# Kernel tuning notes

Hardware: AMD Instinct MI355X
Metric: run time of the kernel (lower is better)

The kernel has to match this reference:

```python
import jax, jax.numpy as jnp
import numpy as np

HEADS = 16
EPS = 1e-6

def _rmsnorm(x, g):
    # x: (..., d); norm = ||x||_2 * d^-0.5 (matches torch.norm-based RMSNorm)
    d = x.shape[-1]
    nrm = jnp.linalg.norm(x, axis=-1, keepdims=True) * (d ** -0.5)
    return x / (nrm + EPS) * g

def _rope(x, cos, sin):
    # x: (b,n,h,d) -> complex pairs over last dim; cos/sin: (1,n,1,d//2)
    b, n, h, d = x.shape
    xr = x.reshape(b, n, h, d // 2, 2)
    re, im = xr[..., 0], xr[..., 1]
    out_re = re * cos - im * sin
    out_im = re * sin + im * cos
    return jnp.stack([out_re, out_im], axis=-1).reshape(b, n, h, d)

def setup_inputs() -> dict:
    key = jax.random.key(0)
    ks = jax.random.split(key, 8)
    b, n, dim = 4, 4096, 1024
    d = dim // HEADS
    x = jax.random.normal(ks[0], (b, n, dim), dtype=jnp.float32)
    # rope freqs as cos/sin of random angles (broadcast shape 1,n,1,d//2)
    ang = jax.random.uniform(ks[1], (1, n, 1, d // 2), dtype=jnp.float32) * (2 * np.pi)
    freqs_cos = jnp.cos(ang)
    freqs_sin = jnp.sin(ang)
    sc = dim ** -0.5
    w_qkv = jax.random.normal(ks[2], (dim, 3 * dim), dtype=jnp.float32) * sc
    g_q = jnp.ones((d,), dtype=jnp.float32)
    g_k = jnp.ones((d,), dtype=jnp.float32)
    w_proj = jax.random.normal(ks[3], (dim, dim), dtype=jnp.float32) * sc
    b_proj = jnp.zeros((dim,), dtype=jnp.float32)
    return {"x": x, "freqs_cos": freqs_cos, "freqs_sin": freqs_sin,
            "w_qkv": w_qkv, "g_q": g_q, "g_k": g_k,
            "w_proj": w_proj, "b_proj": b_proj}

def reference(x, freqs_cos, freqs_sin, w_qkv, g_q, g_k, w_proj, b_proj):
    b, n, dim = x.shape
    h = HEADS
    d = dim // h
    scale = d ** -0.5
    qkv = x @ w_qkv  # (b,n,3*dim)
    q, k, v = jnp.split(qkv, 3, axis=-1)
    q = q.reshape(b, n, h, d)
    k = k.reshape(b, n, h, d)
    v = v.reshape(b, n, h, d)
    q = _rmsnorm(q, g_q)
    k = _rmsnorm(k, g_k)
    q = _rope(q, freqs_cos, freqs_sin)
    k = _rope(k, freqs_cos, freqs_sin)
    # per-token head-mixing attention: (b,n,h,h)
    attn = jnp.einsum('bnhd,bngd->bnhg', q, k) * scale
    attn = jax.nn.softmax(attn, axis=-1)
    out = jnp.einsum('bnhg,bngd->bnhd', attn, v).reshape(b, n, dim)
    return out @ w_proj + b_proj
```

## Files before the change

### kernel.cpp

```cpp
#include <hip/hip_runtime.h>
#include <hip/hip_bf16.h>
#include <stddef.h>

#define NTOK   16384
#define SEQN   4096
#define DIM    1024
#define K3     3072
#define HEADS  16
#define HD     64

typedef __attribute__((ext_vector_type(8))) short short8;
typedef __attribute__((ext_vector_type(4))) float float4v;

static __device__ __forceinline__ unsigned short f32_to_bf16_bits(float f) {
    unsigned u = __float_as_uint(f);
    unsigned r = u + 0x7fffu + ((u >> 16) & 1u);
    return (unsigned short)(r >> 16);
}
static __device__ __forceinline__ float bf16_bits_to_f32(unsigned short h) {
    return __uint_as_float(((unsigned)h) << 16);
}

typedef const void __attribute__((address_space(1)))* gas_ptr;
typedef void __attribute__((address_space(3)))* las_ptr;
static __device__ __forceinline__ void gload_lds16(const unsigned short* g,
                                                   unsigned short* l) {
    __builtin_amdgcn_global_load_lds((gas_ptr)g, (las_ptr)l, 16, 0, 0);
}

__global__ void cvt_f32_bf16(const float4* __restrict__ in,
                             ushort4* __restrict__ out, int n4) {
    int i = blockIdx.x * blockDim.x + threadIdx.x;
    if (i < n4) {
        float4 v = in[i];
        ushort4 o;
        o.x = f32_to_bf16_bits(v.x);
        o.y = f32_to_bf16_bits(v.y);
        o.z = f32_to_bf16_bits(v.z);
        o.w = f32_to_bf16_bits(v.w);
        out[i] = o;
    }
}

__global__ void transpose_cvt(const float* __restrict__ in,
                              unsigned short* __restrict__ out,
                              int K, int N) {
    __shared__ float t[32][33];
    int n0 = blockIdx.x * 32, k0 = blockIdx.y * 32;
    int tx = threadIdx.x, ty = threadIdx.y;
    #pragma unroll
    for (int r = ty; r < 32; r += 8)
        t[r][tx] = in[(size_t)(k0 + r) * N + n0 + tx];
    __syncthreads();
    #pragma unroll
    for (int r = ty; r < 32; r += 8)
        out[(size_t)(n0 + r) * K + k0 + tx] = f32_to_bf16_bits(t[tx][r]);
}

template<int WITH_BIAS>
__global__ __launch_bounds__(256) void gemm_bf16_128(
    const unsigned short* __restrict__ A,
    const unsigned short* __restrict__ Bt,
    void* __restrict__ Cout,
    const float* __restrict__ bias,
    int M, int N, int K)
{
    __shared__ unsigned short As[128][32];
    __shared__ unsigned short Bs[128][32];

    const int tid  = threadIdx.x;
    const int wave = tid >> 6;
    const int lane = tid & 63;
    const int quad = lane >> 4;
    const int l16  = lane & 15;
    const int waveM = (wave & 1) * 64;
    const int waveN = (wave >> 1) * 64;
    const int rowBase = blockIdx.y * 128;
    const int colBase = blockIdx.x * 128;

    float4v acc[4][4];
    #pragma unroll
    for (int i = 0; i < 4; i++)
        #pragma unroll
        for (int j = 0; j < 4; j++)
            acc[i][j] = (float4v)0.0f;

    const int lrow = lane >> 2;
    const int lcol = (lane & 3) * 8;
    const unsigned short* gA = A  + (size_t)(rowBase + wave * 32 + lrow) * K + lcol;
    const unsigned short* gB = Bt + (size_t)(colBase + wave * 32 + lrow) * K + lcol;
    unsigned short* lA0 = &As[wave * 32][0];
    unsigned short* lA1 = &As[wave * 32 + 16][0];
    unsigned short* lB0 = &Bs[wave * 32][0];
    unsigned short* lB1 = &Bs[wave * 32 + 16][0];
    const size_t k16 = (size_t)16 * K;

    for (int k0 = 0; k0 < K; k0 += 32) {
        __syncthreads();
        gload_lds16(gA + k0,        lA0);
        gload_lds16(gA + k0 + k16,  lA1);
        gload_lds16(gB + k0,        lB0);
        gload_lds16(gB + k0 + k16,  lB1);
        __syncthreads();

        short8 af[4], bf[4];
        #pragma unroll
        for (int i = 0; i < 4; i++)
            af[i] = *(const short8*)&As[waveM + i * 16 + l16][quad * 8];
        #pragma unroll
        for (int j = 0; j < 4; j++)
            bf[j] = *(const short8*)&Bs[waveN + j * 16 + l16][quad * 8];

        #pragma unroll
        for (int i = 0; i < 4; i++)
            #pragma unroll
            for (int j = 0; j < 4; j++)
                acc[i][j] = __builtin_amdgcn_mfma_f32_16x16x32_bf16(
                                af[i], bf[j], acc[i][j], 0, 0, 0);
    }

    #pragma unroll
    for (int i = 0; i < 4; i++) {
        #pragma unroll
        for (int j = 0; j < 4; j++) {
            const int col = colBase + waveN + j * 16 + l16;
            #pragma unroll
            for (int r = 0; r < 4; r++) {
                const int row = rowBase + waveM + i * 16 + quad * 4 + r;
                float v = acc[i][j][r];
                if (WITH_BIAS) {
                    ((float*)Cout)[(size_t)row * N + col] = v + bias[col];
                } else {
                    ((unsigned short*)Cout)[(size_t)row * N + col] =
                        f32_to_bf16_bits(v);
                }
            }
        }
    }
}

__global__ __launch_bounds__(256) void attn_tok(
    const unsigned short* __restrict__ qkv,
    const float* __restrict__ fcos,
    const float* __restrict__ fsin,
    const float* __restrict__ gq,
    const float* __restrict__ gk,
    unsigned short* __restrict__ outb)
{
    __shared__ float qs[16][68];
    __shared__ float ks[16][68];
    __shared__ float vs[16][68];
    __shared__ float Ps[16][17];

    const int tok = blockIdx.x;
    const int tid = threadIdx.x;
    const int n   = tok & (SEQN - 1);
    const int h   = tid >> 4;
    const int l   = tid & 15;
    const int d0  = l * 4;

    const unsigned short* base = qkv + (size_t)tok * K3;
    ushort4 qu = *(const ushort4*)(base + tid * 4);
    ushort4 ku = *(const ushort4*)(base + DIM + tid * 4);
    ushort4 vu = *(const ushort4*)(base + 2 * DIM + tid * 4);

    float qx = bf16_bits_to_f32(qu.x), qy = bf16_bits_to_f32(qu.y),
          qz = bf16_bits_to_f32(qu.z), qw = bf16_bits_to_f32(qu.w);
    float kx = bf16_bits_to_f32(ku.x), ky = bf16_bits_to_f32(ku.y),
          kz = bf16_bits_to_f32(ku.z), kw = bf16_bits_to_f32(ku.w);
    float vx = bf16_bits_to_f32(vu.x), vy = bf16_bits_to_f32(vu.y),
          vz = bf16_bits_to_f32(vu.z), vw = bf16_bits_to_f32(vu.w);

    *(float4*)&vs[h][d0] = make_float4(vx, vy, vz, vw);

    float ssq = qx * qx + qy * qy + qz * qz + qw * qw;
    float ssk = kx * kx + ky * ky + kz * kz + kw * kw;
    #pragma unroll
    for (int o = 1; o < 16; o <<= 1) {
        ssq += __shfl_xor(ssq, o);
        ssk += __shfl_xor(ssk, o);
    }
    const float sq = 1.0f / (sqrtf(ssq) * 0.125f + 1e-6f);
    const float sk = 1.0f / (sqrtf(ssk) * 0.125f + 1e-6f);

    float4 g4q = *(const float4*)(gq + d0);
    float4 g4k = *(const float4*)(gk + d0);
    float qa = qx * sq * g4q.x, qb = qy * sq * g4q.y,
          qc = qz * sq * g4q.z, qd = qw * sq * g4q.w;
    float ka = kx * sk * g4k.x, kb = ky * sk * g4k.y,
          kc = kz * sk * g4k.z, kd = kw * sk * g4k.w;

    const int pi = n * (HD / 2) + l * 2;
    float c0 = fcos[pi],     s0 = fsin[pi];
    float c1 = fcos[pi + 1], s1 = fsin[pi + 1];
    *(float4*)&qs[h][d0] = make_float4(qa * c0 - qb * s0, qa * s0 + qb * c0,
                                       qc * c1 - qd * s1, qc * s1 + qd * c1);
    *(float4*)&ks[h][d0] = make_float4(ka * c0 - kb * s0, ka * s0 + kb * c0,
                                       kc * c1 - kd * s1, kc * s1 + kd * c1);
    __syncthreads();

    float s = 0.f;
    const float4* qrow = (const float4*)&qs[h][0];
    const float4* krow = (const float4*)&ks[l][0];
    #pragma unroll
    for (int t = 0; t < 16; t++) {
        float4 a = qrow[t], b = krow[t];
        s += a.x * b.x + a.y * b.y + a.z * b.z + a.w * b.w;
    }
    s *= 0.125f;

    float m = s;
    #pragma unroll
    for (int o = 1; o < 16; o <<= 1) m = fmaxf(m, __shfl_xor(m, o));
    float e = __expf(s - m);
    float sum = e;
    #pragma unroll
    for (int o = 1; o < 16; o <<= 1) sum += __shfl_xor(sum, o);
    Ps[h][l] = e / sum;
    __syncthreads();

    float ox = 0.f, oy = 0.f, oz = 0.f, ow = 0.f;
    #pragma unroll
    for (int g = 0; g < 16; g++) {
        float p = Ps[h][g];
        float4 vv = *(const float4*)&vs[g][d0];
        ox += p * vv.x; oy += p * vv.y; oz += p * vv.z; ow += p * vv.w;
    }
    ushort4 ob;
    ob.x = f32_to_bf16_bits(ox);
    ob.y = f32_to_bf16_bits(oy);
    ob.z = f32_to_bf16_bits(oz);
    ob.w = f32_to_bf16_bits(ow);
    *(ushort4*)(outb + (size_t)tok * DIM + tid * 4) = ob;
}

extern "C" void kernel_launch(void* const* d_in, const int* in_sizes, int n_in,
                              void* d_out, int out_size, void* d_ws, size_t ws_size,
                              hipStream_t stream) {
    const float* x      = (const float*)d_in[0];
    const float* fcos   = (const float*)d_in[1];
    const float* fsin   = (const float*)d_in[2];
    const float* w_qkv  = (const float*)d_in[3];
    const float* g_q    = (const float*)d_in[4];
    const float* g_k    = (const float*)d_in[5];
    const float* w_proj = (const float*)d_in[6];
    const float* b_proj = (const float*)d_in[7];
    float* out = (float*)d_out;

    char* ws = (char*)d_ws;
    unsigned short* xb      = (unsigned short*)(ws);
    unsigned short* wqkvT   = (unsigned short*)(ws + 33554432);
    unsigned short* wprojT  = (unsigned short*)(ws + 39845888);
    unsigned short* qkv     = (unsigned short*)(ws + 41943040);
    unsigned short* attnout = (unsigned short*)(ws + 142606336);
    (void)ws_size; (void)in_sizes; (void)n_in; (void)out_size;

    {
        int n4 = (NTOK * DIM) / 4;
        cvt_f32_bf16<<<(n4 + 255) / 256, 256, 0, stream>>>(
            (const float4*)x, (ushort4*)xb, n4);
        transpose_cvt<<<dim3(K3 / 32, DIM / 32), dim3(32, 8), 0, stream>>>(
            w_qkv, wqkvT, DIM, K3);
        transpose_cvt<<<dim3(DIM / 32, DIM / 32), dim3(32, 8), 0, stream>>>(
            w_proj, wprojT, DIM, DIM);
    }
    gemm_bf16_128<0><<<dim3(K3 / 128, NTOK / 128), 256, 0, stream>>>(
        xb, wqkvT, (void*)qkv, nullptr, NTOK, K3, DIM);
    attn_tok<<<NTOK, 256, 0, stream>>>(qkv, fcos, fsin, g_q, g_k, attnout);
    gemm_bf16_128<1><<<dim3(DIM / 128, NTOK / 128), 256, 0, stream>>>(
        attnout, wprojT, (void*)out, b_proj, NTOK, DIM, DIM);
}
```

Baseline: 381.1 us.

## Restructure per-token attention to one wavefront per token with register dot products

Rewrites the head-mixing attention kernel so each 64-lane wavefront handles one token and four tokens share a block. Each lane holds a 16-element slice of one head's q/k/v in registers, loaded with wide 16-byte accesses. Scores are computed as partial dot products reduced with cross-lane shuffles, and softmax runs in registers. This removes block-wide barriers and the probability staging buffer. The cost is higher register use per thread, and it relies on wave-level ordering of LDS accesses instead of explicit synchronisation.

```diff
diff --git a/kernel.cpp b/kernel.cpp
--- a/kernel.cpp
+++ b/kernel.cpp
@@ -17,8 +17,14 @@
     unsigned r = u + 0x7fffu + ((u >> 16) & 1u);
     return (unsigned short)(r >> 16);
 }
-static __device__ __forceinline__ float bf16_bits_to_f32(unsigned short h) {
-    return __uint_as_float(((unsigned)h) << 16);
+static __device__ __forceinline__ unsigned pack_bf16x2(float lo, float hi) {
+    return (unsigned)f32_to_bf16_bits(lo) | ((unsigned)f32_to_bf16_bits(hi) << 16);
+}
+static __device__ __forceinline__ void unpack_bf16x8(uint4 u, float* f) {
+    f[0] = __uint_as_float(u.x << 16); f[1] = __uint_as_float(u.x & 0xffff0000u);
+    f[2] = __uint_as_float(u.y << 16); f[3] = __uint_as_float(u.y & 0xffff0000u);
+    f[4] = __uint_as_float(u.z << 16); f[5] = __uint_as_float(u.z & 0xffff0000u);
+    f[6] = __uint_as_float(u.w << 16); f[7] = __uint_as_float(u.w & 0xffff0000u);
 }
 
 typedef const void __attribute__((address_space(1)))* gas_ptr;
@@ -147,91 +153,129 @@
     const float* __restrict__ gk,
     unsigned short* __restrict__ outb)
 {
-    __shared__ float qs[16][68];
-    __shared__ float ks[16][68];
-    __shared__ float vs[16][68];
-    __shared__ float Ps[16][17];
-
-    const int tok = blockIdx.x;
-    const int tid = threadIdx.x;
-    const int n   = tok & (SEQN - 1);
-    const int h   = tid >> 4;
-    const int l   = tid & 15;
-    const int d0  = l * 4;
-
-    const unsigned short* base = qkv + (size_t)tok * K3;
-    ushort4 qu = *(const ushort4*)(base + tid * 4);
-    ushort4 ku = *(const ushort4*)(base + DIM + tid * 4);
-    ushort4 vu = *(const ushort4*)(base + 2 * DIM + tid * 4);
-
-    float qx = bf16_bits_to_f32(qu.x), qy = bf16_bits_to_f32(qu.y),
-          qz = bf16_bits_to_f32(qu.z), qw = bf16_bits_to_f32(qu.w);
-    float kx = bf16_bits_to_f32(ku.x), ky = bf16_bits_to_f32(ku.y),
-          kz = bf16_bits_to_f32(ku.z), kw = bf16_bits_to_f32(ku.w);
-    float vx = bf16_bits_to_f32(vu.x), vy = bf16_bits_to_f32(vu.y),
-          vz = bf16_bits_to_f32(vu.z), vw = bf16_bits_to_f32(vu.w);
-
-    *(float4*)&vs[h][d0] = make_float4(vx, vy, vz, vw);
-
-    float ssq = qx * qx + qy * qy + qz * qz + qw * qw;
-    float ssk = kx * kx + ky * ky + kz * kz + kw * kw;
-    #pragma unroll
-    for (int o = 1; o < 16; o <<= 1) {
-        ssq += __shfl_xor(ssq, o);
-        ssk += __shfl_xor(ssk, o);
-    }
+    __shared__ float kl[4][16][68];
+    __shared__ float vl[4][16][68];
+
+    const int tid  = threadIdx.x;
+    const int wv   = tid >> 6;
+    const int lane = tid & 63;
+    const int h    = lane & 15;
+    const int p    = lane >> 4;
+    const int tok  = blockIdx.x * 4 + wv;
+    const int n    = tok & (SEQN - 1);
+
+    const unsigned short* base = qkv + (size_t)tok * K3 + h * 64 + p * 16;
+    uint4 qr0 = *(const uint4*)(base);
+    uint4 qr1 = *(const uint4*)(base + 8);
+    uint4 kr0 = *(const uint4*)(base + DIM);
+    uint4 kr1 = *(const uint4*)(base + DIM + 8);
+    uint4 vr0 = *(const uint4*)(base + 2 * DIM);
+    uint4 vr1 = *(const uint4*)(base + 2 * DIM + 8);
+
+    float q[16], k[16], v[16];
+    unpack_bf16x8(qr0, q); unpack_bf16x8(qr1, q + 8);
+    unpack_bf16x8(kr0, k); unpack_bf16x8(kr1, k + 8);
+    unpack_bf16x8(vr0, v); unpack_bf16x8(vr1, v + 8);
+
+    float ssq = 0.f, ssk = 0.f;
+    #pragma unroll
+    for (int i = 0; i < 16; i++) { ssq += q[i] * q[i]; ssk += k[i] * k[i]; }
+    ssq += __shfl_xor(ssq, 16); ssq += __shfl_xor(ssq, 32);
+    ssk += __shfl_xor(ssk, 16); ssk += __shfl_xor(ssk, 32);
     const float sq = 1.0f / (sqrtf(ssq) * 0.125f + 1e-6f);
     const float sk = 1.0f / (sqrtf(ssk) * 0.125f + 1e-6f);
 
-    float4 g4q = *(const float4*)(gq + d0);
-    float4 g4k = *(const float4*)(gk + d0);
-    float qa = qx * sq * g4q.x, qb = qy * sq * g4q.y,
-          qc = qz * sq * g4q.z, qd = qw * sq * g4q.w;
-    float ka = kx * sk * g4k.x, kb = ky * sk * g4k.y,
-          kc = kz * sk * g4k.z, kd = kw * sk * g4k.w;
-
-    const int pi = n * (HD / 2) + l * 2;
-    float c0 = fcos[pi],     s0 = fsin[pi];
-    float c1 = fcos[pi + 1], s1 = fsin[pi + 1];
-    *(float4*)&qs[h][d0] = make_float4(qa * c0 - qb * s0, qa * s0 + qb * c0,
-                                       qc * c1 - qd * s1, qc * s1 + qd * c1);
-    *(float4*)&ks[h][d0] = make_float4(ka * c0 - kb * s0, ka * s0 + kb * c0,
-                                       kc * c1 - kd * s1, kc * s1 + kd * c1);
-    __syncthreads();
-
-    float s = 0.f;
-    const float4* qrow = (const float4*)&qs[h][0];
-    const float4* krow = (const float4*)&ks[l][0];
-    #pragma unroll
-    for (int t = 0; t < 16; t++) {
-        float4 a = qrow[t], b = krow[t];
-        s += a.x * b.x + a.y * b.y + a.z * b.z + a.w * b.w;
-    }
-    s *= 0.125f;
-
-    float m = s;
-    #pragma unroll
-    for (int o = 1; o < 16; o <<= 1) m = fmaxf(m, __shfl_xor(m, o));
-    float e = __expf(s - m);
-    float sum = e;
-    #pragma unroll
-    for (int o = 1; o < 16; o <<= 1) sum += __shfl_xor(sum, o);
-    Ps[h][l] = e / sum;
-    __syncthreads();
-
-    float ox = 0.f, oy = 0.f, oz = 0.f, ow = 0.f;
+    #pragma unroll
+    for (int c = 0; c < 4; c++) {
+        float4 gg = *(const float4*)(gq + p * 16 + c * 4);
+        float4 gh = *(const float4*)(gk + p * 16 + c * 4);
+        q[c*4+0] *= sq * gg.x; q[c*4+1] *= sq * gg.y;
+        q[c*4+2] *= sq * gg.z; q[c*4+3] *= sq * gg.w;
+        k[c*4+0] *= sk * gh.x; k[c*4+1] *= sk * gh.y;
+        k[c*4+2] *= sk * gh.z; k[c*4+3] *= sk * gh.w;
+    }
+
+    {
+        const float* cb = fcos + n * 32 + p * 8;
+        const float* sb = fsin + n * 32 + p * 8;
+        float4 c0 = *(const float4*)cb, c1 = *(const float4*)(cb + 4);
+        float4 s0 = *(const float4*)sb, s1 = *(const float4*)(sb + 4);
+        float cs[8] = {c0.x,c0.y,c0.z,c0.w,c1.x,c1.y,c1.z,c1.w};
+        float sn[8] = {s0.x,s0.y,s0.z,s0.w,s1.x,s1.y,s1.z,s1.w};
+        #pragma unroll
+        for (int j = 0; j < 8; j++) {
+            float re = q[2*j], im = q[2*j+1];
+            q[2*j]   = re * cs[j] - im * sn[j];
+            q[2*j+1] = re * sn[j] + im * cs[j];
+            re = k[2*j]; im = k[2*j+1];
+            k[2*j]   = re * cs[j] - im * sn[j];
+            k[2*j+1] = re * sn[j] + im * cs[j];
+        }
+    }
+
+    {
+        float* krow = &kl[wv][h][p * 16];
+        float* vrow = &vl[wv][h][p * 16];
+        #pragma unroll
+        for (int c = 0; c < 4; c++) {
+            *(float4*)(krow + c*4) = make_float4(k[c*4], k[c*4+1], k[c*4+2], k[c*4+3]);
+            *(float4*)(vrow + c*4) = make_float4(v[c*4], v[c*4+1], v[c*4+2], v[c*4+3]);
+        }
+    }
+
+    float s[16];
     #pragma unroll
     for (int g = 0; g < 16; g++) {
-        float p = Ps[h][g];
-        float4 vv = *(const float4*)&vs[g][d0];
-        ox += p * vv.x; oy += p * vv.y; oz += p * vv.z; ow += p * vv.w;
-    }
-    ushort4 ob;
-    ob.x = f32_to_bf16_bits(ox);
-    ob.y = f32_to_bf16_bits(oy);
-    ob.z = f32_to_bf16_bits(oz);
-    ob.w = f32_to_bf16_bits(ow);
-    *(ushort4*)(outb + (size_t)tok * DIM + tid * 4) = ob;
+        const float* kg = &kl[wv][g][p * 16];
+        float4 a0 = *(const float4*)(kg);
+        float4 a1 = *(const float4*)(kg + 4);
+        float4 a2 = *(const float4*)(kg + 8);
+        float4 a3 = *(const float4*)(kg + 12);
+        s[g] = q[0]*a0.x + q[1]*a0.y + q[2]*a0.z + q[3]*a0.w
+             + q[4]*a1.x + q[5]*a1.y + q[6]*a1.z + q[7]*a1.w
+             + q[8]*a2.x + q[9]*a2.y + q[10]*a2.z + q[11]*a2.w
+             + q[12]*a3.x + q[13]*a3.y + q[14]*a3.z + q[15]*a3.w;
+    }
+    #pragma unroll
+    for (int g = 0; g < 16; g++) {
+        s[g] += __shfl_xor(s[g], 16);
+        s[g] += __shfl_xor(s[g], 32);
+        s[g] *= 0.125f;
+    }
+
+    float m = s[0];
+    #pragma unroll
+    for (int g = 1; g < 16; g++) m = fmaxf(m, s[g]);
+    float sum = 0.f;
+    #pragma unroll
+    for (int g = 0; g < 16; g++) { s[g] = __expf(s[g] - m); sum += s[g]; }
+    const float inv = 1.0f / sum;
+
+    float o[16];
+    #pragma unroll
+    for (int i = 0; i < 16; i++) o[i] = 0.f;
+    #pragma unroll
+    for (int g = 0; g < 16; g++) {
+        const float pg = s[g] * inv;
+        const float* vg = &vl[wv][g][p * 16];
+        float4 b0 = *(const float4*)(vg);
+        float4 b1 = *(const float4*)(vg + 4);
+        float4 b2 = *(const float4*)(vg + 8);
+        float4 b3 = *(const float4*)(vg + 12);
+        o[0]  += pg * b0.x; o[1]  += pg * b0.y; o[2]  += pg * b0.z; o[3]  += pg * b0.w;
+        o[4]  += pg * b1.x; o[5]  += pg * b1.y; o[6]  += pg * b1.z; o[7]  += pg * b1.w;
+        o[8]  += pg * b2.x; o[9]  += pg * b2.y; o[10] += pg * b2.z; o[11] += pg * b2.w;
+        o[12] += pg * b3.x; o[13] += pg * b3.y; o[14] += pg * b3.z; o[15] += pg * b3.w;
+    }
+
+    uint4 r0, r1;
+    r0.x = pack_bf16x2(o[0],  o[1]);  r0.y = pack_bf16x2(o[2],  o[3]);
+    r0.z = pack_bf16x2(o[4],  o[5]);  r0.w = pack_bf16x2(o[6],  o[7]);
+    r1.x = pack_bf16x2(o[8],  o[9]);  r1.y = pack_bf16x2(o[10], o[11]);
+    r1.z = pack_bf16x2(o[12], o[13]); r1.w = pack_bf16x2(o[14], o[15]);
+    unsigned short* ob = outb + (size_t)tok * DIM + h * 64 + p * 16;
+    *(uint4*)(ob)     = r0;
+    *(uint4*)(ob + 8) = r1;
 }
 
 extern "C" void kernel_launch(void* const* d_in, const int* in_sizes, int n_in,
@@ -266,7 +310,7 @@
     }
     gemm_bf16_128<0><<<dim3(K3 / 128, NTOK / 128), 256, 0, stream>>>(
         xb, wqkvT, (void*)qkv, nullptr, NTOK, K3, DIM);
-    attn_tok<<<NTOK, 256, 0, stream>>>(qkv, fcos, fsin, g_q, g_k, attnout);
+    attn_tok<<<NTOK / 4, 256, 0, stream>>>(qkv, fcos, fsin, g_q, g_k, attnout);
     gemm_bf16_128<1><<<dim3(DIM / 128, NTOK / 128), 256, 0, stream>>>(
         attnout, wprojT, (void*)out, b_proj, NTOK, DIM, DIM);
 }
```

After: 381.0 us. Within noise of the previous version (-0.0%).
